# Kernel optimization log

Hardware: AMD Instinct MI355X
Metric: run time of the kernel (lower is better)

The kernel has to match this reference:

```python
import jax, jax.numpy as jnp
import numpy as np

B, S, D, H, L, K = 16, 512, 256, 8, 4, 16
N, E, NE = B * S, 65536, 32768
DFF = 2 * D
HD = D // H


def _layer_norm(x, g, b):
    mu = jnp.mean(x, axis=-1, keepdims=True)
    var = jnp.mean(jnp.square(x - mu), axis=-1, keepdims=True)
    return (x - mu) / jnp.sqrt(var + 1e-5) * g + b


def setup_inputs() -> dict:
    key = jax.random.key(0)
    ks = iter(jax.random.split(key, 32))
    p = lambda shape: jax.random.normal(next(ks), shape, dtype=jnp.float32) * 0.02
    inp = {
        "node_embedding": jax.random.normal(next(ks), (N, D), dtype=jnp.float32),
        "edge_embedding": jax.random.normal(next(ks), (E, D), dtype=jnp.float32),
        "incidence": jax.random.randint(next(ks), (2, E), 0, N),
        "src_key_padding_mask": jnp.zeros((B, S), dtype=bool),
        "edges_neg": jax.random.randint(next(ks), (NE, 2), 0, N),
        "edges_pos": jax.random.randint(next(ks), (NE, 2), 0, N),
        # ConcatenateLinear(D, D, D): y = x1 @ W1^T + x2 @ W2^T + b
        "msg_w1": p((D, D)), "msg_w2": p((D, D)), "msg_b": p((D,)),
        "pos_table": p((S, D)),
        # per-layer transformer params, stacked on leading L axis
        "in_proj_w": p((L, 3 * D, D)), "in_proj_b": p((L, 3 * D)),
        "out_w": p((L, D, D)), "out_b": p((L, D)),
        "ln1_g": jnp.ones((L, D), jnp.float32), "ln1_b": jnp.zeros((L, D), jnp.float32),
        "ff_w1": p((L, DFF, D)), "ff_b1": p((L, DFF)),
        "ff_w2": p((L, D, DFF)), "ff_b2": p((L, D)),
        "ln2_g": jnp.ones((L, D), jnp.float32), "ln2_b": jnp.zeros((L, D), jnp.float32),
        "pe_w": p((1, D)), "pe_b": p((1,)),
        "pt_w": p((K, D)), "pt_b": p((K,)),
    }
    return inp


def reference(node_embedding, edge_embedding, incidence, src_key_padding_mask,
              edges_neg, edges_pos, msg_w1, msg_w2, msg_b, pos_table,
              in_proj_w, in_proj_b, out_w, out_b, ln1_g, ln1_b,
              ff_w1, ff_b1, ff_w2, ff_b2, ln2_g, ln2_b,
              pe_w, pe_b, pt_w, pt_b):
    # --- aggregate_by_incidence: gather -> ConcatenateLinear -> scatter-add ---
    msgs = (node_embedding[incidence[1]] @ msg_w1.T
            + edge_embedding @ msg_w2.T + msg_b)            # [E, D]
    agreg = jnp.zeros_like(node_embedding).at[incidence[0]].add(msgs)

    # positional encoding tiled over the batch (positions = arange(lMax))
    x = node_embedding + agreg + jnp.tile(pos_table, (B, 1))
    x = x.reshape(B, S, D)

    mask_bias = jnp.where(src_key_padding_mask, -1e9, 0.0)[:, None, None, :]  # [B,1,1,S]
    scale = 1.0 / jnp.sqrt(jnp.float32(HD))

    # post-norm TransformerEncoder (dropout=0 at eval), relu FFN
    for i in range(L):
        wq, wk, wv = jnp.split(in_proj_w[i], 3, axis=0)
        bq, bk, bv = jnp.split(in_proj_b[i], 3, axis=0)
        q = (x @ wq.T + bq).reshape(B, S, H, HD)
        k = (x @ wk.T + bk).reshape(B, S, H, HD)
        v = (x @ wv.T + bv).reshape(B, S, H, HD)
        scores = jnp.einsum('bqhd,bkhd->bhqk', q, k) * scale + mask_bias
        a = jax.nn.softmax(scores, axis=-1)
        o = jnp.einsum('bhqk,bkhd->bqhd', a, v).reshape(B, S, D)
        o = o @ out_w[i].T + out_b[i]
        x = _layer_norm(x + o, ln1_g[i], ln1_b[i])
        h = jax.nn.relu(x @ ff_w1[i].T + ff_b1[i]) @ ff_w2[i].T + ff_b2[i]
        x = _layer_norm(x + h, ln2_g[i], ln2_b[i])

    # --- representation_final_edges: gather pairs, elementwise product ---
    flat = x.reshape(B * S, D)
    rep_pos = flat[edges_pos[:, 0]] * flat[edges_pos[:, 1]]
    rep_neg = flat[edges_neg[:, 0]] * flat[edges_neg[:, 1]]

    pred_pos = rep_pos @ pe_w.T + pe_b      # [NE, 1]
    pred_neg = rep_neg @ pe_w.T + pe_b      # [NE, 1]
    pred_type = rep_pos @ pt_w.T + pt_b     # [NE, K]
    return (pred_pos, pred_neg, pred_type)
```

## Files before the change

kernel.cpp:

```cpp
#include <hip/hip_runtime.h>
#include <hip/hip_bf16.h>

#define B_  16
#define S_  512
#define D_  256
#define H_  8
#define L_  4
#define K_  16
#define N_  (B_ * S_)
#define E_  65536
#define NE_ 32768
#define DFF_ 512
#define HD_ 32

typedef __attribute__((ext_vector_type(8))) __bf16 bf16x8;
typedef __attribute__((ext_vector_type(4))) __bf16 bf16x4;
typedef __attribute__((ext_vector_type(4))) float f32x4;

__device__ __forceinline__ void gl2lds16(const void* g, void* l) {
    __builtin_amdgcn_global_load_lds(
        (const __attribute__((address_space(1))) unsigned int*)g,
        (__attribute__((address_space(3))) unsigned int*)l, 16, 0, 0);
}

#define QSCALE 0.17677669529663688f

__global__ __launch_bounds__(256) void convert_all(
    const float* __restrict__ ipw, __bf16* __restrict__ ipw_bf,
    const float* __restrict__ ow,  __bf16* __restrict__ ow_bf,
    const float* __restrict__ fw1, __bf16* __restrict__ fw1_bf,
    const float* __restrict__ fw2, __bf16* __restrict__ fw2_bf,
    const float* __restrict__ mw1, const float* __restrict__ mw2,
    __bf16* __restrict__ wcat_bf,
    const float* __restrict__ ptw, const float* __restrict__ pew,
    __bf16* __restrict__ wp_bf,
    const float* __restrict__ ipb, float* __restrict__ ipb_s,
    int* __restrict__ cnt)
{
    int blk = blockIdx.x;
    if (blk < 768) {
        size_t i = ((size_t)blk * 256 + threadIdx.x) * 4;
        int row = (int)((i >> 8) % 768);
        float sc = (row < 256) ? QSCALE : 1.0f;
        float4 v = *(const float4*)(ipw + i);
        bf16x4 o = {(__bf16)(v.x * sc), (__bf16)(v.y * sc),
                    (__bf16)(v.z * sc), (__bf16)(v.w * sc)};
        *(bf16x4*)(ipw_bf + i) = o;
    } else if (blk < 2048) {
        const float* src; __bf16* dst; int base;
        if      (blk < 1024)  { src = ow;   dst = ow_bf;   base = blk - 768; }
        else if (blk < 1536)  { src = fw1;  dst = fw1_bf;  base = blk - 1024; }
        else                  { src = fw2;  dst = fw2_bf;  base = blk - 1536; }
        size_t i = ((size_t)base * 256 + threadIdx.x) * 4;
        float4 v = *(const float4*)(src + i);
        bf16x4 o = {(__bf16)v.x, (__bf16)v.y, (__bf16)v.z, (__bf16)v.w};
        *(bf16x4*)(dst + i) = o;
    } else if (blk < 2176) {
        int isw2 = blk >= 2112;
        int base = blk - (isw2 ? 2112 : 2048);
        const float* src = isw2 ? mw2 : mw1;
        size_t i = ((size_t)base * 256 + threadIdx.x) * 4;
        int row = i >> 8, col = i & 255;
        float4 v = *(const float4*)(src + i);
        bf16x4 o = {(__bf16)v.x, (__bf16)v.y, (__bf16)v.z, (__bf16)v.w};
        *(bf16x4*)(wcat_bf + (size_t)row * 512 + (isw2 ? 256 : 0) + col) = o;
    } else if (blk < 2184) {
        int base = blk - 2176;
        size_t i = ((size_t)base * 256 + threadIdx.x) * 4;
        int row = i >> 8, col = i & 255;
        float4 v = make_float4(0.f, 0.f, 0.f, 0.f);
        if (row < 16)       v = *(const float4*)(ptw + row * 256 + col);
        else if (row == 16) v = *(const float4*)(pew + col);
        bf16x4 o = {(__bf16)v.x, (__bf16)v.y, (__bf16)v.z, (__bf16)v.w};
        *(bf16x4*)(wp_bf + i) = o;
    } else if (blk < 2187) {
        int base = blk - 2184;
        size_t i = ((size_t)base * 256 + threadIdx.x) * 4;
        if (i < 3072) {
            float sc = ((i % 768) < 256) ? QSCALE : 1.0f;
            float4 v = *(const float4*)(ipb + i);
            *(float4*)(ipb_s + i) = make_float4(v.x * sc, v.y * sc, v.z * sc, v.w * sc);
        }
    } else {
        int base = blk - 2187;
        int4* p = (int4*)(cnt + ((size_t)base * 256 + threadIdx.x) * 4);
        *p = make_int4(0, 0, 0, 0);
    }
}

__global__ __launch_bounds__(256) void hist_kernel(
    const int* __restrict__ inc, int* __restrict__ cnt)
{
    int e = blockIdx.x * 256 + threadIdx.x;
    atomicAdd(&cnt[inc[e]], 1);
}

__global__ __launch_bounds__(256) void scan_kernel(
    const int* __restrict__ cnt, int* __restrict__ row_ptr, int* __restrict__ ofs)
{
    __shared__ int part[256];
    int t = threadIdx.x;
    int base = t * 32, sum = 0;
    int local[32];
    #pragma unroll
    for (int j = 0; j < 32; ++j) { local[j] = cnt[base + j]; sum += local[j]; }
    part[t] = sum;
    __syncthreads();
    #pragma unroll
    for (int off = 1; off < 256; off <<= 1) {
        int other = (t >= off) ? part[t - off] : 0;
        __syncthreads();
        part[t] += other;
        __syncthreads();
    }
    int run = part[t] - sum;
    for (int j = 0; j < 32; ++j) {
        row_ptr[base + j] = run;
        ofs[base + j] = run;
        run += local[j];
    }
    if (t == 255) row_ptr[8192] = run;
}

__global__ __launch_bounds__(256) void fill_kernel(
    const int* __restrict__ inc, int* __restrict__ ofs, int* __restrict__ elist)
{
    int e = blockIdx.x * 256 + threadIdx.x;
    int pos = atomicAdd(&ofs[inc[e]], 1);
    elist[pos] = e;
}

__global__ __launch_bounds__(256) void csr_gather(
    const float* __restrict__ node, const float* __restrict__ edge,
    const int* __restrict__ inc, const int* __restrict__ row_ptr,
    const int* __restrict__ elist, __bf16* __restrict__ G)
{
    int n = blockIdx.x * 4 + (threadIdx.x >> 6);
    int lane = threadIdx.x & 63;
    int s = row_ptr[n], epos = row_ptr[n + 1];
    float4 an = {0.f, 0.f, 0.f, 0.f}, ae = {0.f, 0.f, 0.f, 0.f};
    int i = s;
    for (; i + 2 <= epos; i += 2) {
        int e0 = elist[i], e1 = elist[i + 1];
        int s0 = inc[E_ + e0], s1 = inc[E_ + e1];
        float4 nv0 = *(const float4*)(node + (size_t)s0 * 256 + lane * 4);
        float4 ev0 = *(const float4*)(edge + (size_t)e0 * 256 + lane * 4);
        float4 nv1 = *(const float4*)(node + (size_t)s1 * 256 + lane * 4);
        float4 ev1 = *(const float4*)(edge + (size_t)e1 * 256 + lane * 4);
        an.x += nv0.x + nv1.x; an.y += nv0.y + nv1.y;
        an.z += nv0.z + nv1.z; an.w += nv0.w + nv1.w;
        ae.x += ev0.x + ev1.x; ae.y += ev0.y + ev1.y;
        ae.z += ev0.z + ev1.z; ae.w += ev0.w + ev1.w;
    }
    if (i < epos) {
        int e0 = elist[i];
        int s0 = inc[E_ + e0];
        float4 nv0 = *(const float4*)(node + (size_t)s0 * 256 + lane * 4);
        float4 ev0 = *(const float4*)(edge + (size_t)e0 * 256 + lane * 4);
        an.x += nv0.x; an.y += nv0.y; an.z += nv0.z; an.w += nv0.w;
        ae.x += ev0.x; ae.y += ev0.y; ae.z += ev0.z; ae.w += ev0.w;
    }
    __bf16* g = G + (size_t)n * 512 + lane * 4;
    bf16x4 bn = {(__bf16)an.x, (__bf16)an.y, (__bf16)an.z, (__bf16)an.w};
    bf16x4 be = {(__bf16)ae.x, (__bf16)ae.y, (__bf16)ae.z, (__bf16)ae.w};
    *(bf16x4*)g = bn;
    *(bf16x4*)(g + 256) = be;
}

template <typename OutT>
__global__ __launch_bounds__(256) void gemm_mfma(
    const __bf16* __restrict__ A, const __bf16* __restrict__ Bw,
    const float* __restrict__ bias, OutT* __restrict__ C,
    int M, int N, int Kd, int relu)
{
    __shared__ __bf16 As0[64 * 32], As1[64 * 32];
    __shared__ __bf16 Bs0[128 * 32], Bs1[128 * 32];
    int tid = threadIdx.x;
    int m0 = blockIdx.y * 64, n0 = blockIdx.x * 128;
    int w = tid >> 6, lane = tid & 63, quad = lane >> 4, r16 = lane & 15;
    int wr = w >> 1, wc = w & 1;

    int lr = tid >> 2, lc = (tid & 3) * 8;
    const __bf16* ag  = A  + (size_t)(m0 + lr) * Kd + lc;
    const __bf16* bg0 = Bw + (size_t)(n0 + lr) * Kd + lc;
    const __bf16* bg1 = bg0 + (size_t)64 * Kd;

    f32x4 acc[2][4] = {};

    for (int k0 = 0; k0 < Kd; k0 += 64) {
        __syncthreads();
        gl2lds16(ag + k0,        As0 + tid * 8);
        gl2lds16(ag + k0 + 32,   As1 + tid * 8);
        gl2lds16(bg0 + k0,       Bs0 + tid * 8);
        gl2lds16(bg1 + k0,       Bs0 + 2048 + tid * 8);
        gl2lds16(bg0 + k0 + 32,  Bs1 + tid * 8);
        gl2lds16(bg1 + k0 + 32,  Bs1 + 2048 + tid * 8);
        __syncthreads();

        #pragma unroll
        for (int kh = 0; kh < 2; ++kh) {
            const __bf16* Asr = kh ? As1 : As0;
            const __bf16* Bsr = kh ? Bs1 : Bs0;
            bf16x8 af[2], bfr[4];
            #pragma unroll
            for (int mt = 0; mt < 2; ++mt)
                af[mt] = *(const bf16x8*)(Asr + (wr * 32 + mt * 16 + r16) * 32 + quad * 8);
            #pragma unroll
            for (int nt = 0; nt < 4; ++nt)
                bfr[nt] = *(const bf16x8*)(Bsr + (wc * 64 + nt * 16 + r16) * 32 + quad * 8);
            #pragma unroll
            for (int mt = 0; mt < 2; ++mt)
                #pragma unroll
                for (int nt = 0; nt < 4; ++nt)
                    acc[mt][nt] = __builtin_amdgcn_mfma_f32_16x16x32_bf16(
                        af[mt], bfr[nt], acc[mt][nt], 0, 0, 0);
        }
    }

    #pragma unroll
    for (int nt = 0; nt < 4; ++nt) {
        int n = n0 + wc * 64 + nt * 16 + r16;
        float bv = bias[n];
        #pragma unroll
        for (int mt = 0; mt < 2; ++mt) {
            #pragma unroll
            for (int reg = 0; reg < 4; ++reg) {
                int m = m0 + wr * 32 + mt * 16 + quad * 4 + reg;
                float v = acc[mt][nt][reg] + bv;
                if (relu) v = fmaxf(v, 0.f);
                C[(size_t)m * N + n] = (OutT)v;
            }
        }
    }
}

__global__ __launch_bounds__(256) void agreg_gemm(
    const __bf16* __restrict__ G, const __bf16* __restrict__ Wc,
    const int* __restrict__ row_ptr, const float* __restrict__ mb,
    const float* __restrict__ node, const float* __restrict__ pos,
    float* __restrict__ xo, __bf16* __restrict__ xo_bf)
{
    __shared__ __bf16 As0[32 * 32], As1[32 * 32];
    __shared__ __bf16 Bs0[128 * 32], Bs1[128 * 32];
    int tid = threadIdx.x;
    int m0 = blockIdx.y * 32, n0 = blockIdx.x * 128;
    int w = tid >> 6, lane = tid & 63, quad = lane >> 4, r16 = lane & 15;
    int wr = w >> 1, wc = w & 1;

    int lr = tid >> 2, lc = (tid & 3) * 8;
    const __bf16* ag  = G  + (size_t)(m0 + (tid >> 2 & 31)) * 512 + lc;
    const __bf16* bg0 = Wc + (size_t)(n0 + lr) * 512 + lc;
    const __bf16* bg1 = bg0 + (size_t)64 * 512;

    f32x4 acc[4] = {};

    for (int k0 = 0; k0 < 512; k0 += 64) {
        __syncthreads();
        if (tid < 128) {
            gl2lds16(ag + k0,      As0 + tid * 8);
            gl2lds16(ag + k0 + 32, As1 + tid * 8);
        }
        gl2lds16(bg0 + k0,       Bs0 + tid * 8);
        gl2lds16(bg1 + k0,       Bs0 + 2048 + tid * 8);
        gl2lds16(bg0 + k0 + 32,  Bs1 + tid * 8);
        gl2lds16(bg1 + k0 + 32,  Bs1 + 2048 + tid * 8);
        __syncthreads();

        #pragma unroll
        for (int kh = 0; kh < 2; ++kh) {
            const __bf16* Asr = kh ? As1 : As0;
            const __bf16* Bsr = kh ? Bs1 : Bs0;
            bf16x8 af = *(const bf16x8*)(Asr + (wr * 16 + r16) * 32 + quad * 8);
            #pragma unroll
            for (int nt = 0; nt < 4; ++nt) {
                bf16x8 bfr = *(const bf16x8*)(Bsr + (wc * 64 + nt * 16 + r16) * 32 + quad * 8);
                acc[nt] = __builtin_amdgcn_mfma_f32_16x16x32_bf16(af, bfr, acc[nt], 0, 0, 0);
            }
        }
    }

    #pragma unroll
    for (int nt = 0; nt < 4; ++nt) {
        int n = n0 + wc * 64 + nt * 16 + r16;
        float mbv = mb[n];
        #pragma unroll
        for (int reg = 0; reg < 4; ++reg) {
            int m = m0 + wr * 16 + quad * 4 + reg;
            float deg = (float)(row_ptr[m + 1] - row_ptr[m]);
            float v = acc[nt][reg] + deg * mbv
                    + node[(size_t)m * 256 + n] + pos[(size_t)(m & 511) * 256 + n];
            xo[(size_t)m * 256 + n] = v;
            xo_bf[(size_t)m * 256 + n] = (__bf16)v;
        }
    }
}

__global__ __launch_bounds__(256) void tail_fused(
    const __bf16* __restrict__ A,
    const __bf16* __restrict__ Wo,
    const float* __restrict__ ob,
    const float* __restrict__ res,
    const float* __restrict__ g1, const float* __restrict__ b1,
    const __bf16* __restrict__ W1,
    const float* __restrict__ fb1,
    const __bf16* __restrict__ W2,
    const float* __restrict__ fb2,
    const float* __restrict__ g2, const float* __restrict__ b2,
    float* __restrict__ xo, __bf16* __restrict__ xo_bf, int wx32)
{
    __shared__ __bf16 Bs[512 * 32];
    __shared__ __bf16 As0[16 * 32], As1[16 * 32];
    __shared__ __bf16 x1s[16 * 264];
    __shared__ __bf16 hs[16 * 520];
    __shared__ float redS[4][16], redQ[4][16];

    int tid = threadIdx.x;
    int m0 = blockIdx.x * 16;
    int w = tid >> 6, lane = tid & 63, quad = lane >> 4, r16 = lane & 15;

    f32x4 acc[4] = {};
    for (int k0 = 0; k0 < 256; k0 += 64) {
        __syncthreads();
        if (tid < 64) {
            const __bf16* ap = A + (size_t)(m0 + (tid >> 2)) * 256 + (tid & 3) * 8;
            gl2lds16(ap + k0,      As0 + tid * 8);
            gl2lds16(ap + k0 + 32, As1 + tid * 8);
        }
        #pragma unroll
        for (int c = 0; c < 4; ++c) {
            const __bf16* wp = Wo + (size_t)(c * 64 + (tid >> 2)) * 256 + (tid & 3) * 8;
            gl2lds16(wp + k0,      Bs + c * 2048 + tid * 8);
            gl2lds16(wp + k0 + 32, Bs + 8192 + c * 2048 + tid * 8);
        }
        __syncthreads();

        #pragma unroll
        for (int kh = 0; kh < 2; ++kh) {
            const __bf16* Asr = kh ? As1 : As0;
            const __bf16* Bsr = Bs + kh * 8192;
            bf16x8 af = *(const bf16x8*)(Asr + r16 * 32 + quad * 8);
            #pragma unroll
            for (int nt = 0; nt < 4; ++nt) {
                bf16x8 bfr = *(const bf16x8*)(Bsr + (w * 64 + nt * 16 + r16) * 32 + quad * 8);
                acc[nt] = __builtin_amdgcn_mfma_f32_16x16x32_bf16(af, bfr, acc[nt], 0, 0, 0);
            }
        }
    }

    float vv1[4][4];
    {
        float ls[4], lq[4];
        #pragma unroll
        for (int reg = 0; reg < 4; ++reg) {
            int m = m0 + quad * 4 + reg;
            float s = 0.f, q = 0.f;
            #pragma unroll
            for (int nt = 0; nt < 4; ++nt) {
                int col = w * 64 + nt * 16 + r16;
                float val = acc[nt][reg] + ob[col] + res[(size_t)m * 256 + col];
                vv1[reg][nt] = val;
                s += val; q += val * val;
            }
            #pragma unroll
            for (int off = 1; off < 16; off <<= 1) {
                s += __shfl_xor(s, off);
                q += __shfl_xor(q, off);
            }
            ls[reg] = s; lq[reg] = q;
        }
        if (r16 == 0) {
            #pragma unroll
            for (int reg = 0; reg < 4; ++reg) {
                int r = quad * 4 + reg;
                redS[w][r] = ls[reg];
                redQ[w][r] = lq[reg];
            }
        }
        __syncthreads();
        #pragma unroll
        for (int reg = 0; reg < 4; ++reg) {
            int r = quad * 4 + reg;
            float s = redS[0][r] + redS[1][r] + redS[2][r] + redS[3][r];
            float q = redQ[0][r] + redQ[1][r] + redQ[2][r] + redQ[3][r];
            float mu = s * (1.f / 256.f);
            float var = q * (1.f / 256.f) - mu * mu;
            float rstd = rsqrtf(var + 1e-5f);
            #pragma unroll
            for (int nt = 0; nt < 4; ++nt) {
                int col = w * 64 + nt * 16 + r16;
                float val = (vv1[reg][nt] - mu) * rstd * g1[col] + b1[col];
                vv1[reg][nt] = val;
                x1s[r * 264 + col] = (__bf16)val;
            }
        }
    }

    f32x4 hacc[8] = {};
    for (int k0 = 0; k0 < 256; k0 += 32) {
        __syncthreads();
        {
            const __bf16* wp = W1 + (size_t)(tid >> 2) * 256 + (tid & 3) * 8 + k0;
            #pragma unroll
            for (int j = 0; j < 8; ++j)
                gl2lds16(wp + (size_t)j * 64 * 256, Bs + j * 2048 + tid * 8);
        }
        __syncthreads();
        bf16x8 af = *(const bf16x8*)(x1s + r16 * 264 + k0 + quad * 8);
        #pragma unroll
        for (int nt = 0; nt < 8; ++nt) {
            bf16x8 bfr = *(const bf16x8*)(Bs + (w * 128 + nt * 16 + r16) * 32 + quad * 8);
            hacc[nt] = __builtin_amdgcn_mfma_f32_16x16x32_bf16(af, bfr, hacc[nt], 0, 0, 0);
        }
    }
    #pragma unroll
    for (int nt = 0; nt < 8; ++nt) {
        int col = w * 128 + nt * 16 + r16;
        float bb = fb1[col];
        #pragma unroll
        for (int reg = 0; reg < 4; ++reg) {
            float v = fmaxf(hacc[nt][reg] + bb, 0.f);
            hs[(quad * 4 + reg) * 520 + col] = (__bf16)v;
        }
    }

    f32x4 cacc[4] = {};
    for (int k0 = 0; k0 < 512; k0 += 64) {
        __syncthreads();
        #pragma unroll
        for (int c = 0; c < 4; ++c) {
            const __bf16* wp = W2 + (size_t)(c * 64 + (tid >> 2)) * 512 + (tid & 3) * 8;
            gl2lds16(wp + k0,      Bs + c * 2048 + tid * 8);
            gl2lds16(wp + k0 + 32, Bs + 8192 + c * 2048 + tid * 8);
        }
        __syncthreads();
        #pragma unroll
        for (int kh = 0; kh < 2; ++kh) {
            const __bf16* Bsr = Bs + kh * 8192;
            bf16x8 af = *(const bf16x8*)(hs + r16 * 520 + k0 + kh * 32 + quad * 8);
            #pragma unroll
            for (int nt = 0; nt < 4; ++nt) {
                bf16x8 bfr = *(const bf16x8*)(Bsr + (w * 64 + nt * 16 + r16) * 32 + quad * 8);
                cacc[nt] = __builtin_amdgcn_mfma_f32_16x16x32_bf16(af, bfr, cacc[nt], 0, 0, 0);
            }
        }
    }

    {
        float vvc[4][4];
        float ls[4], lq[4];
        #pragma unroll
        for (int reg = 0; reg < 4; ++reg) {
            float s = 0.f, q = 0.f;
            #pragma unroll
            for (int nt = 0; nt < 4; ++nt) {
                int col = w * 64 + nt * 16 + r16;
                float val = cacc[nt][reg] + fb2[col] + vv1[reg][nt];
                vvc[reg][nt] = val;
                s += val; q += val * val;
            }
            #pragma unroll
            for (int off = 1; off < 16; off <<= 1) {
                s += __shfl_xor(s, off);
                q += __shfl_xor(q, off);
            }
            ls[reg] = s; lq[reg] = q;
        }
        __syncthreads();
        if (r16 == 0) {
            #pragma unroll
            for (int reg = 0; reg < 4; ++reg) {
                int r = quad * 4 + reg;
                redS[w][r] = ls[reg];
                redQ[w][r] = lq[reg];
            }
        }
        __syncthreads();
        #pragma unroll
        for (int reg = 0; reg < 4; ++reg) {
            int r = quad * 4 + reg;
            int m = m0 + r;
            float s = redS[0][r] + redS[1][r] + redS[2][r] + redS[3][r];
            float q = redQ[0][r] + redQ[1][r] + redQ[2][r] + redQ[3][r];
            float mu = s * (1.f / 256.f);
            float var = q * (1.f / 256.f) - mu * mu;
            float rstd = rsqrtf(var + 1e-5f);
            #pragma unroll
            for (int nt = 0; nt < 4; ++nt) {
                int col = w * 64 + nt * 16 + r16;
                float val = (vvc[reg][nt] - mu) * rstd * g2[col] + b2[col];
                if (wx32) xo[(size_t)m * 256 + col] = val;
                xo_bf[(size_t)m * 256 + col] = (__bf16)val;
            }
        }
    }
}

#define VS 72
#define PS 72

__global__ __launch_bounds__(256) void attn_mfma_kernel(
    const __bf16* __restrict__ qkv, __bf16* __restrict__ o)
{
    __shared__ __bf16 Vt[2][32 * VS];
    __shared__ __bf16 Ps[4][16 * PS];

    int tid  = threadIdx.x;
    int w    = tid >> 6, lane = tid & 63;
    int quad = lane >> 4, r16 = lane & 15;
    int qt = blockIdx.x;
    int bh = blockIdx.y;
    int b = bh >> 3, h = bh & 7;
    int base = b * S_;
    int q0 = qt * 64;

    bf16x8 qa = *(const bf16x8*)(
        qkv + (size_t)(base + q0 + w * 16 + r16) * 768 + h * 32 + quad * 8);

    int kp  = tid & 31;
    int cch = (tid >> 5) & 3;
    int jh  = tid >> 7;
    const __bf16* vbase = qkv + (size_t)base * 768 + 512 + h * 32 + cch * 8;
    const __bf16* kbase = qkv + (size_t)base * 768 + 256 + h * 32 + quad * 8;

    bf16x8 va  = *(const bf16x8*)(vbase + (size_t)(2 * kp) * 768);
    bf16x8 vb2 = *(const bf16x8*)(vbase + (size_t)(2 * kp + 1) * 768);
    bf16x8 kb[4], kbn[4];
    #pragma unroll
    for (int t = 0; t < 4; ++t)
        kbn[t] = *(const bf16x8*)(kbase + (size_t)(t * 16 + r16) * 768);

    f32x4 oacc0 = {0.f, 0.f, 0.f, 0.f};
    f32x4 oacc1 = {0.f, 0.f, 0.f, 0.f};
    float l_i[4] = {0.f, 0.f, 0.f, 0.f};

    for (int kt = 0; kt < 8; ++kt) {
        int buf = kt & 1;
        #pragma unroll
        for (int j = 0; j < 4; ++j) {
            int jj = jh * 4 + j;
            int d = cch * 8 + jj;
            union { __bf16 hh[2]; unsigned int u; } pk;
            pk.hh[0] = va[jj];
            pk.hh[1] = vb2[jj];
            *(unsigned int*)(&Vt[buf][d * VS + 2 * kp]) = pk.u;
        }
        #pragma unroll
        for (int t = 0; t < 4; ++t) kb[t] = kbn[t];
        __syncthreads();

        if (kt < 7) {
            int off = (kt + 1) * 64;
            va  = *(const bf16x8*)(vbase + (size_t)(off + 2 * kp) * 768);
            vb2 = *(const bf16x8*)(vbase + (size_t)(off + 2 * kp + 1) * 768);
            #pragma unroll
            for (int t = 0; t < 4; ++t)
                kbn[t] = *(const bf16x8*)(kbase + (size_t)(off + t * 16 + r16) * 768);
        }

        f32x4 s[4];
        #pragma unroll
        for (int t = 0; t < 4; ++t)
            s[t] = __builtin_amdgcn_mfma_f32_16x16x32_bf16(
                qa, kb[t], (f32x4){0.f, 0.f, 0.f, 0.f}, 0, 0, 0);

        #pragma unroll
        for (int r = 0; r < 4; ++r) {
            float p0 = __expf(s[0][r]), p1 = __expf(s[1][r]);
            float p2 = __expf(s[2][r]), p3 = __expf(s[3][r]);
            l_i[r] += (p0 + p1) + (p2 + p3);
            __bf16* pw = &Ps[w][(quad * 4 + r) * PS + r16];
            pw[0]  = (__bf16)p0;
            pw[16] = (__bf16)p1;
            pw[32] = (__bf16)p2;
            pw[48] = (__bf16)p3;
        }

        #pragma unroll
        for (int c = 0; c < 2; ++c) {
            bf16x8 pa  = *(const bf16x8*)(&Ps[w][r16 * PS + c * 32 + quad * 8]);
            bf16x8 vb0 = *(const bf16x8*)(&Vt[buf][r16 * VS + c * 32 + quad * 8]);
            bf16x8 vb1 = *(const bf16x8*)(&Vt[buf][(16 + r16) * VS + c * 32 + quad * 8]);
            oacc0 = __builtin_amdgcn_mfma_f32_16x16x32_bf16(pa, vb0, oacc0, 0, 0, 0);
            oacc1 = __builtin_amdgcn_mfma_f32_16x16x32_bf16(pa, vb1, oacc1, 0, 0, 0);
        }
    }

    #pragma unroll
    for (int r = 0; r < 4; ++r) {
        float ls = l_i[r];
        #pragma unroll
        for (int off = 1; off < 16; off <<= 1) ls += __shfl_xor(ls, off);
        float inv = 1.0f / ls;
        int q = base + q0 + w * 16 + quad * 4 + r;
        __bf16* op = o + (size_t)q * 256 + h * 32;
        op[r16]      = (__bf16)(oacc0[r] * inv);
        op[16 + r16] = (__bf16)(oacc1[r] * inv);
    }
}

#define PP 264

__global__ __launch_bounds__(256) void pred_mfma(
    const __bf16* __restrict__ xbf, const int* __restrict__ ep,
    const int* __restrict__ en, const __bf16* __restrict__ Wp,
    const float* __restrict__ pe_b, const float* __restrict__ pt_b,
    float* __restrict__ out)
{
    __shared__ __bf16 P[4][16 * PP];
    int tid = threadIdx.x;
    int w = tid >> 6, lane = tid & 63, quad = lane >> 4, r16 = lane & 15;
    int isPos = blockIdx.x < 512;
    int e0 = (blockIdx.x & 511) * 64 + w * 16;
    const int* epair = isPos ? ep : en;

    int half = lane >> 5;
    int col = (lane & 31) * 8;
    #pragma unroll
    for (int j = 0; j < 8; ++j) {
        int je = j * 2 + half;
        int e = e0 + je;
        int a = epair[2 * e], c = epair[2 * e + 1];
        bf16x8 av = *(const bf16x8*)(xbf + (size_t)a * 256 + col);
        bf16x8 cv = *(const bf16x8*)(xbf + (size_t)c * 256 + col);
        bf16x8 pv;
        #pragma unroll
        for (int t = 0; t < 8; ++t)
            pv[t] = (__bf16)((float)av[t] * (float)cv[t]);
        *(bf16x8*)(&P[w][je * PP + col]) = pv;
    }
    __syncthreads();

    f32x4 acc1 = {0.f, 0.f, 0.f, 0.f};
    f32x4 acc2 = {0.f, 0.f, 0.f, 0.f};
    #pragma unroll
    for (int k0 = 0; k0 < 256; k0 += 32) {
        bf16x8 af = *(const bf16x8*)(&P[w][r16 * PP + k0 + quad * 8]);
        bf16x8 b2 = *(const bf16x8*)(Wp + (size_t)(16 + r16) * 256 + k0 + quad * 8);
        acc2 = __builtin_amdgcn_mfma_f32_16x16x32_bf16(af, b2, acc2, 0, 0, 0);
        if (isPos) {
            bf16x8 b1 = *(const bf16x8*)(Wp + (size_t)r16 * 256 + k0 + quad * 8);
            acc1 = __builtin_amdgcn_mfma_f32_16x16x32_bf16(af, b1, acc1, 0, 0, 0);
        }
    }

    float* pred_pos = out;
    float* pred_neg = out + NE_;
    float* pred_type = out + 2 * NE_;
    float peb = pe_b[0];
    if (isPos) {
        float ptbv = pt_b[r16];
        #pragma unroll
        for (int reg = 0; reg < 4; ++reg) {
            int e = e0 + quad * 4 + reg;
            pred_type[(size_t)e * 16 + r16] = acc1[reg] + ptbv;
        }
        if (r16 == 0) {
            #pragma unroll
            for (int reg = 0; reg < 4; ++reg)
                pred_pos[e0 + quad * 4 + reg] = acc2[reg] + peb;
        }
    } else {
        if (r16 == 0) {
            #pragma unroll
            for (int reg = 0; reg < 4; ++reg)
                pred_neg[e0 + quad * 4 + reg] = acc2[reg] + peb;
        }
    }
}

extern "C" void kernel_launch(void* const* d_in, const int* in_sizes, int n_in,
                              void* d_out, int out_size, void* d_ws, size_t ws_size,
                              hipStream_t stream)
{
    const float* node_emb  = (const float*)d_in[0];
    const float* edge_emb  = (const float*)d_in[1];
    const int*   incidence = (const int*)d_in[2];
    const int*   edges_neg = (const int*)d_in[4];
    const int*   edges_pos = (const int*)d_in[5];
    const float* msg_w1    = (const float*)d_in[6];
    const float* msg_w2    = (const float*)d_in[7];
    const float* msg_b     = (const float*)d_in[8];
    const float* pos_table = (const float*)d_in[9];
    const float* in_proj_w = (const float*)d_in[10];
    const float* in_proj_b = (const float*)d_in[11];
    const float* out_w     = (const float*)d_in[12];
    const float* out_b     = (const float*)d_in[13];
    const float* ln1_g     = (const float*)d_in[14];
    const float* ln1_b     = (const float*)d_in[15];
    const float* ff_w1     = (const float*)d_in[16];
    const float* ff_b1     = (const float*)d_in[17];
    const float* ff_w2     = (const float*)d_in[18];
    const float* ff_b2     = (const float*)d_in[19];
    const float* ln2_g     = (const float*)d_in[20];
    const float* ln2_b     = (const float*)d_in[21];
    const float* pe_w      = (const float*)d_in[22];
    const float* pe_b      = (const float*)d_in[23];
    const float* pt_w      = (const float*)d_in[24];
    const float* pt_b      = (const float*)d_in[25];

    float*  x       = (float*)d_ws;
    __bf16* x_bf    = (__bf16*)(x + (size_t)N_ * D_);
    __bf16* ipw_bf  = x_bf + (size_t)N_ * D_;
    __bf16* ow_bf   = ipw_bf + 786432;
    __bf16* fw1_bf  = ow_bf + 262144;
    __bf16* fw2_bf  = fw1_bf + 524288;
    __bf16* wcat_bf = fw2_bf + 524288;
    __bf16* wp_bf   = wcat_bf + 131072;
    float*  ipb_s   = (float*)(wp_bf + 8192);
    float*  scratch = ipb_s + 3072;
    int*    cnt     = (int*)scratch;
    int*    row_ptr = cnt + 8192;
    int*    ofs     = row_ptr + 8200;
    int*    elist   = ofs + 8192;
    __bf16* qkv_bf = (__bf16*)scratch;
    __bf16* o_bf   = qkv_bf + (size_t)N_ * 768;
    __bf16* G_bf   = (__bf16*)(scratch + 6291456);

    convert_all<<<2195, 256, 0, stream>>>(
        in_proj_w, ipw_bf, out_w, ow_bf, ff_w1, fw1_bf, ff_w2, fw2_bf,
        msg_w1, msg_w2, wcat_bf, pt_w, pe_w, wp_bf, in_proj_b, ipb_s, cnt);

    hist_kernel<<<E_ / 256, 256, 0, stream>>>(incidence, cnt);
    scan_kernel<<<1, 256, 0, stream>>>(cnt, row_ptr, ofs);
    fill_kernel<<<E_ / 256, 256, 0, stream>>>(incidence, ofs, elist);

    csr_gather<<<N_ / 4, 256, 0, stream>>>(
        node_emb, edge_emb, incidence, row_ptr, elist, G_bf);
    agreg_gemm<<<dim3(2, N_ / 32), 256, 0, stream>>>(
        G_bf, wcat_bf, row_ptr, msg_b, node_emb, pos_table, x, x_bf);

    for (int li = 0; li < L_; ++li) {
        gemm_mfma<__bf16><<<dim3(768 / 128, N_ / 64), 256, 0, stream>>>(
            x_bf, ipw_bf + (size_t)li * 768 * 256, ipb_s + li * 768,
            qkv_bf, N_, 768, 256, 0);
        attn_mfma_kernel<<<dim3(S_ / 64, B_ * H_), 256, 0, stream>>>(qkv_bf, o_bf);
        tail_fused<<<N_ / 16, 256, 0, stream>>>(
            o_bf, ow_bf + (size_t)li * 256 * 256, out_b + li * 256,
            x, ln1_g + li * 256, ln1_b + li * 256,
            fw1_bf + (size_t)li * 512 * 256, ff_b1 + li * 512,
            fw2_bf + (size_t)li * 256 * 512, ff_b2 + li * 256,
            ln2_g + li * 256, ln2_b + li * 256,
            x, x_bf, li == L_ - 1 ? 0 : 1);
    }

    pred_mfma<<<1024, 256, 0, stream>>>(
        x_bf, edges_pos, edges_neg, wp_bf, pe_b, pt_b, (float*)d_out);
}
```

Baseline: 442.2 us.

## Restructure tail_fused to 32-row tiles with 8 waves and direct-register weight loads

The fused out-proj/LN/FFN/LN tail kernel now handles 32 rows per block with 512 threads (8 waves) instead of 16 rows with 256 threads. Weight B-fragments are read straight from global memory into registers instead of being staged through LDS with a barrier per k-step, and the activation tile is loaded once into padded LDS. This removes most of the per-k-step syncs and halves the number of times each block streams the weights relative to rows processed. The cost is uncoalesced, L2-dependent weight fragment loads and more waves contending per block.

```diff
diff --git a/kernel.cpp b/kernel.cpp
--- a/kernel.cpp
+++ b/kernel.cpp
@@ -295,7 +295,7 @@
     }
 }
 
-__global__ __launch_bounds__(256) void tail_fused(
+__global__ __launch_bounds__(512) void tail_fused(
     const __bf16* __restrict__ A,
     const __bf16* __restrict__ Wo,
     const float* __restrict__ ob,
@@ -308,57 +308,58 @@
     const float* __restrict__ g2, const float* __restrict__ b2,
     float* __restrict__ xo, __bf16* __restrict__ xo_bf, int wx32)
 {
-    __shared__ __bf16 Bs[512 * 32];
-    __shared__ __bf16 As0[16 * 32], As1[16 * 32];
-    __shared__ __bf16 x1s[16 * 264];
-    __shared__ __bf16 hs[16 * 520];
-    __shared__ float redS[4][16], redQ[4][16];
+    __shared__ __bf16 As[32 * 264];
+    __shared__ __bf16 x1s[32 * 264];
+    __shared__ __bf16 hs[32 * 520];
+    __shared__ float redS[8][32], redQ[8][32];
 
     int tid = threadIdx.x;
-    int m0 = blockIdx.x * 16;
+    int m0 = blockIdx.x * 32;
     int w = tid >> 6, lane = tid & 63, quad = lane >> 4, r16 = lane & 15;
 
-    f32x4 acc[4] = {};
-    for (int k0 = 0; k0 < 256; k0 += 64) {
-        __syncthreads();
-        if (tid < 64) {
-            const __bf16* ap = A + (size_t)(m0 + (tid >> 2)) * 256 + (tid & 3) * 8;
-            gl2lds16(ap + k0,      As0 + tid * 8);
-            gl2lds16(ap + k0 + 32, As1 + tid * 8);
-        }
-        #pragma unroll
-        for (int c = 0; c < 4; ++c) {
-            const __bf16* wp = Wo + (size_t)(c * 64 + (tid >> 2)) * 256 + (tid & 3) * 8;
-            gl2lds16(wp + k0,      Bs + c * 2048 + tid * 8);
-            gl2lds16(wp + k0 + 32, Bs + 8192 + c * 2048 + tid * 8);
-        }
-        __syncthreads();
-
-        #pragma unroll
-        for (int kh = 0; kh < 2; ++kh) {
-            const __bf16* Asr = kh ? As1 : As0;
-            const __bf16* Bsr = Bs + kh * 8192;
-            bf16x8 af = *(const bf16x8*)(Asr + r16 * 32 + quad * 8);
-            #pragma unroll
-            for (int nt = 0; nt < 4; ++nt) {
-                bf16x8 bfr = *(const bf16x8*)(Bsr + (w * 64 + nt * 16 + r16) * 32 + quad * 8);
-                acc[nt] = __builtin_amdgcn_mfma_f32_16x16x32_bf16(af, bfr, acc[nt], 0, 0, 0);
-            }
-        }
-    }
-
-    float vv1[4][4];
+    #pragma unroll
+    for (int rpt = 0; rpt < 2; ++rpt) {
+        int c = tid + rpt * 512;
+        int row = c >> 5, cc = c & 31;
+        bf16x8 v = *(const bf16x8*)(A + (size_t)(m0 + row) * 256 + cc * 8);
+        *(bf16x8*)(&As[row * 264 + cc * 8]) = v;
+    }
+    __syncthreads();
+
+    f32x4 acc[2][2] = {};
     {
-        float ls[4], lq[4];
+        const __bf16* wp0 = Wo + (size_t)(w * 32 + r16) * 256 + quad * 8;
+        #pragma unroll
+        for (int k0 = 0; k0 < 256; k0 += 32) {
+            bf16x8 af[2], bfr[2];
+            #pragma unroll
+            for (int mt = 0; mt < 2; ++mt)
+                af[mt] = *(const bf16x8*)(&As[(mt * 16 + r16) * 264 + k0 + quad * 8]);
+            #pragma unroll
+            for (int nt = 0; nt < 2; ++nt)
+                bfr[nt] = *(const bf16x8*)(wp0 + (size_t)(nt * 16) * 256 + k0);
+            #pragma unroll
+            for (int mt = 0; mt < 2; ++mt)
+                #pragma unroll
+                for (int nt = 0; nt < 2; ++nt)
+                    acc[mt][nt] = __builtin_amdgcn_mfma_f32_16x16x32_bf16(
+                        af[mt], bfr[nt], acc[mt][nt], 0, 0, 0);
+        }
+    }
+
+    float vv1[2][2][4];
+    #pragma unroll
+    for (int mt = 0; mt < 2; ++mt) {
         #pragma unroll
         for (int reg = 0; reg < 4; ++reg) {
-            int m = m0 + quad * 4 + reg;
+            int r = mt * 16 + quad * 4 + reg;
+            int m = m0 + r;
             float s = 0.f, q = 0.f;
             #pragma unroll
-            for (int nt = 0; nt < 4; ++nt) {
-                int col = w * 64 + nt * 16 + r16;
-                float val = acc[nt][reg] + ob[col] + res[(size_t)m * 256 + col];
-                vv1[reg][nt] = val;
+            for (int nt = 0; nt < 2; ++nt) {
+                int col = w * 32 + nt * 16 + r16;
+                float val = acc[mt][nt][reg] + ob[col] + res[(size_t)m * 256 + col];
+                vv1[mt][nt][reg] = val;
                 s += val; q += val * val;
             }
             #pragma unroll
@@ -366,96 +367,98 @@
                 s += __shfl_xor(s, off);
                 q += __shfl_xor(q, off);
             }
-            ls[reg] = s; lq[reg] = q;
-        }
-        if (r16 == 0) {
-            #pragma unroll
-            for (int reg = 0; reg < 4; ++reg) {
-                int r = quad * 4 + reg;
-                redS[w][r] = ls[reg];
-                redQ[w][r] = lq[reg];
-            }
-        }
-        __syncthreads();
+            if (r16 == 0) { redS[w][r] = s; redQ[w][r] = q; }
+        }
+    }
+    __syncthreads();
+    #pragma unroll
+    for (int mt = 0; mt < 2; ++mt) {
         #pragma unroll
         for (int reg = 0; reg < 4; ++reg) {
-            int r = quad * 4 + reg;
-            float s = redS[0][r] + redS[1][r] + redS[2][r] + redS[3][r];
-            float q = redQ[0][r] + redQ[1][r] + redQ[2][r] + redQ[3][r];
+            int r = mt * 16 + quad * 4 + reg;
+            float s = 0.f, q = 0.f;
+            #pragma unroll
+            for (int ww = 0; ww < 8; ++ww) { s += redS[ww][r]; q += redQ[ww][r]; }
             float mu = s * (1.f / 256.f);
             float var = q * (1.f / 256.f) - mu * mu;
             float rstd = rsqrtf(var + 1e-5f);
             #pragma unroll
+            for (int nt = 0; nt < 2; ++nt) {
+                int col = w * 32 + nt * 16 + r16;
+                float val = (vv1[mt][nt][reg] - mu) * rstd * g1[col] + b1[col];
+                vv1[mt][nt][reg] = val;
+                x1s[r * 264 + col] = (__bf16)val;
+            }
+        }
+    }
+    __syncthreads();
+
+    f32x4 hacc[2][4] = {};
+    {
+        const __bf16* wp1 = W1 + (size_t)(w * 64 + r16) * 256 + quad * 8;
+        #pragma unroll
+        for (int k0 = 0; k0 < 256; k0 += 32) {
+            bf16x8 af[2];
+            #pragma unroll
+            for (int mt = 0; mt < 2; ++mt)
+                af[mt] = *(const bf16x8*)(&x1s[(mt * 16 + r16) * 264 + k0 + quad * 8]);
+            #pragma unroll
             for (int nt = 0; nt < 4; ++nt) {
-                int col = w * 64 + nt * 16 + r16;
-                float val = (vv1[reg][nt] - mu) * rstd * g1[col] + b1[col];
-                vv1[reg][nt] = val;
-                x1s[r * 264 + col] = (__bf16)val;
-            }
-        }
-    }
-
-    f32x4 hacc[8] = {};
-    for (int k0 = 0; k0 < 256; k0 += 32) {
-        __syncthreads();
-        {
-            const __bf16* wp = W1 + (size_t)(tid >> 2) * 256 + (tid & 3) * 8 + k0;
-            #pragma unroll
-            for (int j = 0; j < 8; ++j)
-                gl2lds16(wp + (size_t)j * 64 * 256, Bs + j * 2048 + tid * 8);
-        }
-        __syncthreads();
-        bf16x8 af = *(const bf16x8*)(x1s + r16 * 264 + k0 + quad * 8);
-        #pragma unroll
-        for (int nt = 0; nt < 8; ++nt) {
-            bf16x8 bfr = *(const bf16x8*)(Bs + (w * 128 + nt * 16 + r16) * 32 + quad * 8);
-            hacc[nt] = __builtin_amdgcn_mfma_f32_16x16x32_bf16(af, bfr, hacc[nt], 0, 0, 0);
-        }
-    }
-    #pragma unroll
-    for (int nt = 0; nt < 8; ++nt) {
-        int col = w * 128 + nt * 16 + r16;
+                bf16x8 bfr = *(const bf16x8*)(wp1 + (size_t)(nt * 16) * 256 + k0);
+                #pragma unroll
+                for (int mt = 0; mt < 2; ++mt)
+                    hacc[mt][nt] = __builtin_amdgcn_mfma_f32_16x16x32_bf16(
+                        af[mt], bfr, hacc[mt][nt], 0, 0, 0);
+            }
+        }
+    }
+    #pragma unroll
+    for (int nt = 0; nt < 4; ++nt) {
+        int col = w * 64 + nt * 16 + r16;
         float bb = fb1[col];
         #pragma unroll
+        for (int mt = 0; mt < 2; ++mt)
+            #pragma unroll
+            for (int reg = 0; reg < 4; ++reg) {
+                float v = fmaxf(hacc[mt][nt][reg] + bb, 0.f);
+                hs[(mt * 16 + quad * 4 + reg) * 520 + col] = (__bf16)v;
+            }
+    }
+    __syncthreads();
+
+    f32x4 cacc[2][2] = {};
+    {
+        const __bf16* wp2 = W2 + (size_t)(w * 32 + r16) * 512 + quad * 8;
+        #pragma unroll
+        for (int k0 = 0; k0 < 512; k0 += 32) {
+            bf16x8 af[2], bfr[2];
+            #pragma unroll
+            for (int mt = 0; mt < 2; ++mt)
+                af[mt] = *(const bf16x8*)(&hs[(mt * 16 + r16) * 520 + k0 + quad * 8]);
+            #pragma unroll
+            for (int nt = 0; nt < 2; ++nt)
+                bfr[nt] = *(const bf16x8*)(wp2 + (size_t)(nt * 16) * 512 + k0);
+            #pragma unroll
+            for (int mt = 0; mt < 2; ++mt)
+                #pragma unroll
+                for (int nt = 0; nt < 2; ++nt)
+                    cacc[mt][nt] = __builtin_amdgcn_mfma_f32_16x16x32_bf16(
+                        af[mt], bfr[nt], cacc[mt][nt], 0, 0, 0);
+        }
+    }
+
+    float vvc[2][2][4];
+    #pragma unroll
+    for (int mt = 0; mt < 2; ++mt) {
+        #pragma unroll
         for (int reg = 0; reg < 4; ++reg) {
-            float v = fmaxf(hacc[nt][reg] + bb, 0.f);
-            hs[(quad * 4 + reg) * 520 + col] = (__bf16)v;
-        }
-    }
-
-    f32x4 cacc[4] = {};
-    for (int k0 = 0; k0 < 512; k0 += 64) {
-        __syncthreads();
-        #pragma unroll
-        for (int c = 0; c < 4; ++c) {
-            const __bf16* wp = W2 + (size_t)(c * 64 + (tid >> 2)) * 512 + (tid & 3) * 8;
-            gl2lds16(wp + k0,      Bs + c * 2048 + tid * 8);
-            gl2lds16(wp + k0 + 32, Bs + 8192 + c * 2048 + tid * 8);
-        }
-        __syncthreads();
-        #pragma unroll
-        for (int kh = 0; kh < 2; ++kh) {
-            const __bf16* Bsr = Bs + kh * 8192;
-            bf16x8 af = *(const bf16x8*)(hs + r16 * 520 + k0 + kh * 32 + quad * 8);
-            #pragma unroll
-            for (int nt = 0; nt < 4; ++nt) {
-                bf16x8 bfr = *(const bf16x8*)(Bsr + (w * 64 + nt * 16 + r16) * 32 + quad * 8);
-                cacc[nt] = __builtin_amdgcn_mfma_f32_16x16x32_bf16(af, bfr, cacc[nt], 0, 0, 0);
-            }
-        }
-    }
-
-    {
-        float vvc[4][4];
-        float ls[4], lq[4];
-        #pragma unroll
-        for (int reg = 0; reg < 4; ++reg) {
+            int r = mt * 16 + quad * 4 + reg;
             float s = 0.f, q = 0.f;
             #pragma unroll
-            for (int nt = 0; nt < 4; ++nt) {
-                int col = w * 64 + nt * 16 + r16;
-                float val = cacc[nt][reg] + fb2[col] + vv1[reg][nt];
-                vvc[reg][nt] = val;
+            for (int nt = 0; nt < 2; ++nt) {
+                int col = w * 32 + nt * 16 + r16;
+                float val = cacc[mt][nt][reg] + fb2[col] + vv1[mt][nt][reg];
+                vvc[mt][nt][reg] = val;
                 s += val; q += val * val;
             }
             #pragma unroll
@@ -463,31 +466,26 @@
                 s += __shfl_xor(s, off);
                 q += __shfl_xor(q, off);
             }
-            ls[reg] = s; lq[reg] = q;
-        }
-        __syncthreads();
-        if (r16 == 0) {
-            #pragma unroll
-            for (int reg = 0; reg < 4; ++reg) {
-                int r = quad * 4 + reg;
-                redS[w][r] = ls[reg];
-                redQ[w][r] = lq[reg];
-            }
-        }
-        __syncthreads();
+            if (r16 == 0) { redS[w][r] = s; redQ[w][r] = q; }
+        }
+    }
+    __syncthreads();
+    #pragma unroll
+    for (int mt = 0; mt < 2; ++mt) {
         #pragma unroll
         for (int reg = 0; reg < 4; ++reg) {
-            int r = quad * 4 + reg;
+            int r = mt * 16 + quad * 4 + reg;
             int m = m0 + r;
-            float s = redS[0][r] + redS[1][r] + redS[2][r] + redS[3][r];
-            float q = redQ[0][r] + redQ[1][r] + redQ[2][r] + redQ[3][r];
+            float s = 0.f, q = 0.f;
+            #pragma unroll
+            for (int ww = 0; ww < 8; ++ww) { s += redS[ww][r]; q += redQ[ww][r]; }
             float mu = s * (1.f / 256.f);
             float var = q * (1.f / 256.f) - mu * mu;
             float rstd = rsqrtf(var + 1e-5f);
             #pragma unroll
-            for (int nt = 0; nt < 4; ++nt) {
-                int col = w * 64 + nt * 16 + r16;
-                float val = (vvc[reg][nt] - mu) * rstd * g2[col] + b2[col];
+            for (int nt = 0; nt < 2; ++nt) {
+                int col = w * 32 + nt * 16 + r16;
+                float val = (vvc[mt][nt][reg] - mu) * rstd * g2[col] + b2[col];
                 if (wx32) xo[(size_t)m * 256 + col] = val;
                 xo_bf[(size_t)m * 256 + col] = (__bf16)val;
             }
@@ -734,7 +732,7 @@
             x_bf, ipw_bf + (size_t)li * 768 * 256, ipb_s + li * 768,
             qkv_bf, N_, 768, 256, 0);
         attn_mfma_kernel<<<dim3(S_ / 64, B_ * H_), 256, 0, stream>>>(qkv_bf, o_bf);
-        tail_fused<<<N_ / 16, 256, 0, stream>>>(
+        tail_fused<<<N_ / 32, 512, 0, stream>>>(
             o_bf, ow_bf + (size_t)li * 256 * 256, out_b + li * 256,
             x, ln1_g + li * 256, ln1_b + li * 256,
             fw1_bf + (size_t)li * 512 * 256, ff_b1 + li * 512,
```

Measured after the change: 464.4 us. 1.05x slower.

## Read tail weights directly from global memory instead of staging through LDS

Applied to the files above, without the earlier changes.

In the fused out-proj/LN/FFN tail kernel, the three weight matrices are now loaded as MFMA B-fragments straight from global memory (relying on L2/L1 caching), instead of being staged through a shared LDS buffer. This removes the per-k-step LDS copy and its paired barriers. The A tile is loaded into LDS once up front. LDS use drops, which may raise occupancy, but every block now issues many small uncoalesced global loads with no latency hiding through staging.

```diff
diff --git a/kernel.cpp b/kernel.cpp
--- a/kernel.cpp
+++ b/kernel.cpp
@@ -308,8 +308,7 @@
     const float* __restrict__ g2, const float* __restrict__ b2,
     float* __restrict__ xo, __bf16* __restrict__ xo_bf, int wx32)
 {
-    __shared__ __bf16 Bs[512 * 32];
-    __shared__ __bf16 As0[16 * 32], As1[16 * 32];
+    __shared__ __bf16 As[16 * 264];
     __shared__ __bf16 x1s[16 * 264];
     __shared__ __bf16 hs[16 * 520];
     __shared__ float redS[4][16], redQ[4][16];
@@ -318,30 +317,24 @@
     int m0 = blockIdx.x * 16;
     int w = tid >> 6, lane = tid & 63, quad = lane >> 4, r16 = lane & 15;
 
+    #pragma unroll
+    for (int rpt = 0; rpt < 2; ++rpt) {
+        int c = tid + rpt * 256;
+        int row = c >> 5, cc = c & 31;
+        bf16x8 v = *(const bf16x8*)(A + (size_t)(m0 + row) * 256 + cc * 8);
+        *(bf16x8*)(&As[row * 264 + cc * 8]) = v;
+    }
+    __syncthreads();
+
     f32x4 acc[4] = {};
-    for (int k0 = 0; k0 < 256; k0 += 64) {
-        __syncthreads();
-        if (tid < 64) {
-            const __bf16* ap = A + (size_t)(m0 + (tid >> 2)) * 256 + (tid & 3) * 8;
-            gl2lds16(ap + k0,      As0 + tid * 8);
-            gl2lds16(ap + k0 + 32, As1 + tid * 8);
-        }
-        #pragma unroll
-        for (int c = 0; c < 4; ++c) {
-            const __bf16* wp = Wo + (size_t)(c * 64 + (tid >> 2)) * 256 + (tid & 3) * 8;
-            gl2lds16(wp + k0,      Bs + c * 2048 + tid * 8);
-            gl2lds16(wp + k0 + 32, Bs + 8192 + c * 2048 + tid * 8);
-        }
-        __syncthreads();
-
-        #pragma unroll
-        for (int kh = 0; kh < 2; ++kh) {
-            const __bf16* Asr = kh ? As1 : As0;
-            const __bf16* Bsr = Bs + kh * 8192;
-            bf16x8 af = *(const bf16x8*)(Asr + r16 * 32 + quad * 8);
+    {
+        const __bf16* wp0 = Wo + (size_t)(w * 64 + r16) * 256 + quad * 8;
+        #pragma unroll
+        for (int k0 = 0; k0 < 256; k0 += 32) {
+            bf16x8 af = *(const bf16x8*)(&As[r16 * 264 + k0 + quad * 8]);
             #pragma unroll
             for (int nt = 0; nt < 4; ++nt) {
-                bf16x8 bfr = *(const bf16x8*)(Bsr + (w * 64 + nt * 16 + r16) * 32 + quad * 8);
+                bf16x8 bfr = *(const bf16x8*)(wp0 + (size_t)(nt * 16) * 256 + k0);
                 acc[nt] = __builtin_amdgcn_mfma_f32_16x16x32_bf16(af, bfr, acc[nt], 0, 0, 0);
             }
         }
@@ -394,22 +387,19 @@
             }
         }
     }
+    __syncthreads();
 
     f32x4 hacc[8] = {};
-    for (int k0 = 0; k0 < 256; k0 += 32) {
-        __syncthreads();
-        {
-            const __bf16* wp = W1 + (size_t)(tid >> 2) * 256 + (tid & 3) * 8 + k0;
-            #pragma unroll
-            for (int j = 0; j < 8; ++j)
-                gl2lds16(wp + (size_t)j * 64 * 256, Bs + j * 2048 + tid * 8);
-        }
-        __syncthreads();
-        bf16x8 af = *(const bf16x8*)(x1s + r16 * 264 + k0 + quad * 8);
-        #pragma unroll
-        for (int nt = 0; nt < 8; ++nt) {
-            bf16x8 bfr = *(const bf16x8*)(Bs + (w * 128 + nt * 16 + r16) * 32 + quad * 8);
-            hacc[nt] = __builtin_amdgcn_mfma_f32_16x16x32_bf16(af, bfr, hacc[nt], 0, 0, 0);
+    {
+        const __bf16* wp1 = W1 + (size_t)(w * 128 + r16) * 256 + quad * 8;
+        #pragma unroll
+        for (int k0 = 0; k0 < 256; k0 += 32) {
+            bf16x8 af = *(const bf16x8*)(&x1s[r16 * 264 + k0 + quad * 8]);
+            #pragma unroll
+            for (int nt = 0; nt < 8; ++nt) {
+                bf16x8 bfr = *(const bf16x8*)(wp1 + (size_t)(nt * 16) * 256 + k0);
+                hacc[nt] = __builtin_amdgcn_mfma_f32_16x16x32_bf16(af, bfr, hacc[nt], 0, 0, 0);
+            }
         }
     }
     #pragma unroll
@@ -422,24 +412,17 @@
             hs[(quad * 4 + reg) * 520 + col] = (__bf16)v;
         }
     }
+    __syncthreads();
 
     f32x4 cacc[4] = {};
-    for (int k0 = 0; k0 < 512; k0 += 64) {
-        __syncthreads();
-        #pragma unroll
-        for (int c = 0; c < 4; ++c) {
-            const __bf16* wp = W2 + (size_t)(c * 64 + (tid >> 2)) * 512 + (tid & 3) * 8;
-            gl2lds16(wp + k0,      Bs + c * 2048 + tid * 8);
-            gl2lds16(wp + k0 + 32, Bs + 8192 + c * 2048 + tid * 8);
-        }
-        __syncthreads();
-        #pragma unroll
-        for (int kh = 0; kh < 2; ++kh) {
-            const __bf16* Bsr = Bs + kh * 8192;
-            bf16x8 af = *(const bf16x8*)(hs + r16 * 520 + k0 + kh * 32 + quad * 8);
+    {
+        const __bf16* wp2 = W2 + (size_t)(w * 64 + r16) * 512 + quad * 8;
+        #pragma unroll
+        for (int k0 = 0; k0 < 512; k0 += 32) {
+            bf16x8 af = *(const bf16x8*)(&hs[r16 * 520 + k0 + quad * 8]);
             #pragma unroll
             for (int nt = 0; nt < 4; ++nt) {
-                bf16x8 bfr = *(const bf16x8*)(Bsr + (w * 64 + nt * 16 + r16) * 32 + quad * 8);
+                bf16x8 bfr = *(const bf16x8*)(wp2 + (size_t)(nt * 16) * 512 + k0);
                 cacc[nt] = __builtin_amdgcn_mfma_f32_16x16x32_bf16(af, bfr, cacc[nt], 0, 0, 0);
             }
         }
```

New measurement: 509.4 us. 15.2% more time.
